# Kernel tuning notes

Measured on AMD Instinct MI355X. Metric: run time of the kernel, lower is better.

## Reference

```python
import jax, jax.numpy as jnp
import numpy as np

N_NODES = 50000
N_EDGES = 640000
IN_DIM = 128
HID = 256
OUT = 256
BN_EPS = 1e-5
L2_EPS = 1e-12


def setup_inputs() -> dict:
    key = jax.random.key(0)
    ks = jax.random.split(key, 12)
    x = jax.random.normal(ks[0], (N_NODES, IN_DIM), dtype=jnp.float32)
    edge_index = jax.random.randint(ks[1], (2, N_EDGES), 0, N_NODES, dtype=jnp.int64)
    s0 = 1.0 / np.sqrt(IN_DIM)
    s1 = 1.0 / np.sqrt(HID)
    return {
        "x": x,
        "edge_index": edge_index,
        # SAGEConv layer 0: lin_l (aggregated neighbors, with bias), lin_r (root, no bias)
        "W_l0": jax.random.uniform(ks[2], (IN_DIM, HID), jnp.float32, -s0, s0),
        "b_l0": jax.random.uniform(ks[3], (HID,), jnp.float32, -s0, s0),
        "W_r0": jax.random.uniform(ks[4], (IN_DIM, HID), jnp.float32, -s0, s0),
        # SAGEConv layer 1
        "W_l1": jax.random.uniform(ks[5], (HID, OUT), jnp.float32, -s1, s1),
        "b_l1": jax.random.uniform(ks[6], (OUT,), jnp.float32, -s1, s1),
        "W_r1": jax.random.uniform(ks[7], (HID, OUT), jnp.float32, -s1, s1),
        # BatchNorm1d (eval mode: running stats)
        "bn_gamma": jax.random.uniform(ks[8], (HID,), jnp.float32, 0.5, 1.5),
        "bn_beta": 0.1 * jax.random.normal(ks[9], (HID,), dtype=jnp.float32),
        "bn_mean": 0.1 * jax.random.normal(ks[10], (HID,), dtype=jnp.float32),
        "bn_var": jax.random.uniform(ks[11], (HID,), jnp.float32, 0.5, 1.5),
    }


def _l2norm(v):
    # F.normalize(v, p=2, dim=1)
    n = jnp.sqrt(jnp.sum(v * v, axis=1, keepdims=True))
    return v / jnp.maximum(n, L2_EPS)


def _sage_mean(x, src, dst, W_l, b_l, W_r, n_nodes):
    # mean-aggregate source features at destination nodes (PyG source_to_target)
    msg = x[src]                                   # [E, d] gather
    agg = jax.ops.segment_sum(msg, dst, num_segments=n_nodes)
    cnt = jax.ops.segment_sum(jnp.ones((src.shape[0], 1), x.dtype), dst, num_segments=n_nodes)
    agg = agg / jnp.maximum(cnt, 1.0)
    out = agg @ W_l + b_l + x @ W_r
    return _l2norm(out)                            # SAGEConv(normalize=True)


def reference(x, edge_index, W_l0, b_l0, W_r0, W_l1, b_l1, W_r1,
              bn_gamma, bn_beta, bn_mean, bn_var):
    src, dst = edge_index[0], edge_index[1]
    n = x.shape[0]
    h = _sage_mean(x, src, dst, W_l0, b_l0, W_r0, n)
    # BatchNorm1d in eval mode (dropout is identity in eval)
    h = (h - bn_mean) * (bn_gamma / jnp.sqrt(bn_var + BN_EPS)) + bn_beta
    h = jax.nn.relu(h)
    h = _sage_mean(h, src, dst, W_l1, b_l1, W_r1, n)
    # final F.normalize(x, p=2, dim=1)
    return _l2norm(h)
```

## Files before the change

### kernel.cpp

```cpp
#include <hip/hip_runtime.h>

#define NN 50000

typedef __bf16 bf16x8 __attribute__((ext_vector_type(8)));
typedef float f32x4 __attribute__((ext_vector_type(4)));
typedef float f32x2 __attribute__((ext_vector_type(2)));

__device__ __forceinline__ unsigned short f2bf(float f) {
    unsigned int u = __builtin_bit_cast(unsigned int, f);
    u += 0x7FFF + ((u >> 16) & 1);
    return (unsigned short)(u >> 16);
}
__device__ __forceinline__ float bf2f(unsigned short h) {
    unsigned int u = ((unsigned int)h) << 16;
    return __builtin_bit_cast(float, u);
}
__device__ __forceinline__ unsigned char f2fp8(float f) {
    return (unsigned char)(__builtin_amdgcn_cvt_pk_fp8_f32(f, f, 0, false) & 0xff);
}
__device__ __forceinline__ void gload16(const void* g, void* l) {
    __builtin_amdgcn_global_load_lds(
        (const __attribute__((address_space(1))) unsigned int*)g,
        (__attribute__((address_space(3))) unsigned int*)l, 16, 0, 0);
}

__global__ void init_kernel(const int* __restrict__ ei32, int* __restrict__ flag,
                            int* __restrict__ cnt, int n) {
    if (blockIdx.x == 0) {
        __shared__ int red[256];
        int tid = threadIdx.x;
        int o = 0;
        for (int i = tid; i < 4096; i += 256) o |= ei32[2 * i + 1];
        red[tid] = o;
        __syncthreads();
        for (int s = 128; s > 0; s >>= 1) {
            if (tid < s) red[tid] |= red[tid + s];
            __syncthreads();
        }
        if (tid == 0) *flag = (red[0] == 0) ? 1 : 0;
    } else {
        int i0 = (blockIdx.x - 1) * 1024 + threadIdx.x * 4;
#pragma unroll
        for (int j = 0; j < 4; ++j) {
            int i = i0 + j;
            if (i < n) cnt[i] = 0;
        }
    }
}

__device__ __forceinline__ int load_edge(const void* ei, int is64, long long idx) {
    return is64 ? (int)((const long long*)ei)[idx] : ((const int*)ei)[idx];
}

__global__ void hist_kernel(const void* __restrict__ ei, const int* __restrict__ flag,
                            int* __restrict__ cnt, int E) {
    int e = blockIdx.x * blockDim.x + threadIdx.x;
    if (e >= E) return;
    int is64 = *flag;
    int dst = load_edge(ei, is64, (long long)E + e);
    atomicAdd(&cnt[dst], 1);
}

__global__ void scan_part(const int* __restrict__ cnt, int* __restrict__ bsum, int n) {
    __shared__ int s[256];
    const int tid = threadIdx.x;
    const int i0 = blockIdx.x * 1024 + tid * 4;
    int sum = 0;
#pragma unroll
    for (int j = 0; j < 4; ++j) {
        int i = i0 + j;
        if (i < n) sum += cnt[i];
    }
    s[tid] = sum;
    __syncthreads();
    for (int o = 128; o > 0; o >>= 1) {
        if (tid < o) s[tid] += s[tid + o];
        __syncthreads();
    }
    if (tid == 0) bsum[blockIdx.x] = s[0];
}

__global__ void scan_fin2(const int* __restrict__ cnt, const int* __restrict__ bsum,
                          int* __restrict__ off, int* __restrict__ pos, int n, int nb) {
    __shared__ int s[256];
    __shared__ int base_sh, total_sh;
    const int tid = threadIdx.x;
    if (tid < 64) {
        int v = (tid < nb) ? bsum[tid] : 0;
        int incl = v;
#pragma unroll
        for (int o = 1; o < 64; o <<= 1) {
            int t = __shfl_up(incl, o, 64);
            if (tid >= o) incl += t;
        }
        if (tid == (int)blockIdx.x) base_sh = incl - v;
        if (tid == 63) total_sh = incl;
    }
    const int i0 = blockIdx.x * 1024 + tid * 4;
    int v[4];
    int sum = 0;
#pragma unroll
    for (int j = 0; j < 4; ++j) {
        int i = i0 + j;
        v[j] = (i < n) ? cnt[i] : 0;
        sum += v[j];
    }
    s[tid] = sum;
    __syncthreads();
    for (int o = 1; o < 256; o <<= 1) {
        int t = 0;
        if (tid >= o) t = s[tid - o];
        __syncthreads();
        s[tid] += t;
        __syncthreads();
    }
    int run = base_sh + s[tid] - sum;
#pragma unroll
    for (int j = 0; j < 4; ++j) {
        int i = i0 + j;
        if (i < n) {
            off[i] = run;
            pos[i] = run;
            run += v[j];
        }
    }
    if (blockIdx.x == 0 && tid == 0) off[n] = total_sh;
}

__global__ void fill_kernel(const void* __restrict__ ei, const int* __restrict__ flag,
                            int* __restrict__ pos, int* __restrict__ adj, int E) {
    int e = blockIdx.x * blockDim.x + threadIdx.x;
    if (e >= E) return;
    int is64 = *flag;
    int src = load_edge(ei, is64, e);
    int dst = load_edge(ei, is64, (long long)E + e);
    int p = atomicAdd(&pos[dst], 1);
    adj[p] = src;
}

__global__ void prep_fused(const float* __restrict__ x, unsigned char* __restrict__ xf8,
                           unsigned short* __restrict__ xbf_t,
                           const float* __restrict__ Wl0, const float* __restrict__ Wr0,
                           unsigned short* __restrict__ Wt0,
                           const float* __restrict__ Wl1, const float* __restrict__ Wr1,
                           unsigned short* __restrict__ Wt1, int n4, int NC) {
    int b = blockIdx.x;
    if (b < NC) {
        int i = b * 256 + threadIdx.x;
        if (i >= n4) return;
        float4 v = ((const float4*)x)[i];
        int p8 = __builtin_amdgcn_cvt_pk_fp8_f32(v.x, v.y, 0, false);
        p8 = __builtin_amdgcn_cvt_pk_fp8_f32(v.z, v.w, p8, true);
        ((unsigned int*)xf8)[i] = (unsigned int)p8;
        uint2 o;
        o.x = (unsigned int)f2bf(v.x) | ((unsigned int)f2bf(v.y) << 16);
        o.y = (unsigned int)f2bf(v.z) | ((unsigned int)f2bf(v.w) << 16);
        int r = i >> 5;
        int kk = (i & 31) * 4;
        int ts = kk >> 5, q = (kk >> 3) & 3, e = kk & 7;
        size_t idx = ((size_t)(r >> 6) * 4 + ts) * 2048 + q * 512 + (r & 63) * 8 + e;
        *(uint2*)(xbf_t + idx) = o;
    } else if (b < NC + 256) {
        int c = b - NC;
        for (int k = threadIdx.x; k < 256; k += blockDim.x) {
            float v = (k < 128) ? Wl0[(size_t)k * 256 + c] : Wr0[(size_t)(k - 128) * 256 + c];
            int ks = k >> 5, q = (k >> 3) & 3, e = k & 7;
            Wt0[(size_t)ks * 8192 + q * 2048 + c * 8 + e] = f2bf(v);
        }
    } else {
        int c = b - NC - 256;
        for (int k = threadIdx.x; k < 512; k += blockDim.x) {
            float v = (k < 256) ? Wl1[(size_t)k * 256 + c] : Wr1[(size_t)(k - 256) * 256 + c];
            int ks = k >> 5, q = (k >> 3) & 3, e = k & 7;
            Wt1[(size_t)ks * 8192 + q * 2048 + c * 8 + e] = f2bf(v);
        }
    }
}

__global__ void agg_l0(const unsigned char* __restrict__ feat8, const int* __restrict__ off,
                       const int* __restrict__ adj, unsigned short* __restrict__ out_t, int n) {
    int node = blockIdx.x * 8 + (threadIdx.x >> 5);
    if (node >= n) return;
    const int lane = threadIdx.x & 31;
    const int s = off[node], e = off[node + 1];

    float a0[4] = {}, a1[4] = {}, a2[4] = {}, a3[4] = {};
    const unsigned char* fbase = feat8 + lane * 4;

    auto addrow = [&](float* acc, int src) {
        unsigned int u = *(const unsigned int*)(fbase + (size_t)src * 128);
        f32x2 lo = __builtin_amdgcn_cvt_pk_f32_fp8(u, false);
        f32x2 hi = __builtin_amdgcn_cvt_pk_f32_fp8(u, true);
        acc[0] += lo[0];
        acc[1] += lo[1];
        acc[2] += hi[0];
        acc[3] += hi[1];
    };

    int j = s;
    for (; j + 4 <= e; j += 4) {
        int i0 = adj[j], i1 = adj[j + 1], i2 = adj[j + 2], i3 = adj[j + 3];
        addrow(a0, i0);
        addrow(a1, i1);
        addrow(a2, i2);
        addrow(a3, i3);
    }
    {
        int rem = e - j;
        if (rem > 0) addrow(a0, adj[j]);
        if (rem > 1) addrow(a1, adj[j + 1]);
        if (rem > 2) addrow(a2, adj[j + 2]);
    }

    int deg = e - s;
    float inv = 1.0f / (float)(deg > 0 ? deg : 1);
#pragma unroll
    for (int k = 0; k < 4; ++k) a0[k] = (a0[k] + a1[k] + a2[k] + a3[k]) * inv;

    const int k0 = lane * 4;
    const int ts = k0 >> 5, q = (k0 >> 3) & 3, e8 = k0 & 7;
    size_t idx = ((size_t)(node >> 6) * 4 + ts) * 2048 + q * 512 + (node & 63) * 8 + e8;
    uint2 o;
    o.x = (unsigned int)f2bf(a0[0]) | ((unsigned int)f2bf(a0[1]) << 16);
    o.y = (unsigned int)f2bf(a0[2]) | ((unsigned int)f2bf(a0[3]) << 16);
    *(uint2*)(out_t + idx) = o;
}

__global__ void agg_l1(const unsigned char* __restrict__ feat8, const int* __restrict__ off,
                       const int* __restrict__ adj, unsigned short* __restrict__ out_t, int n) {
    int node = blockIdx.x * 8 + (threadIdx.x >> 5);
    if (node >= n) return;
    const int lane = threadIdx.x & 31;
    const int s = off[node], e = off[node + 1];

    float a0[8] = {}, a1[8] = {}, a2[8] = {}, a3[8] = {};
    const unsigned char* fbase = feat8 + lane * 8;

    auto addrow = [&](float* acc, int src) {
        uint2 u = *(const uint2*)(fbase + (size_t)src * 256);
        f32x2 p0 = __builtin_amdgcn_cvt_pk_f32_fp8(u.x, false);
        f32x2 p1 = __builtin_amdgcn_cvt_pk_f32_fp8(u.x, true);
        f32x2 p2 = __builtin_amdgcn_cvt_pk_f32_fp8(u.y, false);
        f32x2 p3 = __builtin_amdgcn_cvt_pk_f32_fp8(u.y, true);
        acc[0] += p0[0];
        acc[1] += p0[1];
        acc[2] += p1[0];
        acc[3] += p1[1];
        acc[4] += p2[0];
        acc[5] += p2[1];
        acc[6] += p3[0];
        acc[7] += p3[1];
    };

    int j = s;
    for (; j + 4 <= e; j += 4) {
        int i0 = adj[j], i1 = adj[j + 1], i2 = adj[j + 2], i3 = adj[j + 3];
        addrow(a0, i0);
        addrow(a1, i1);
        addrow(a2, i2);
        addrow(a3, i3);
    }
    {
        int rem = e - j;
        if (rem > 0) addrow(a0, adj[j]);
        if (rem > 1) addrow(a1, adj[j + 1]);
        if (rem > 2) addrow(a2, adj[j + 2]);
    }

    int deg = e - s;
    float inv = 1.0f / (float)(deg > 0 ? deg : 1);
#pragma unroll
    for (int k = 0; k < 8; ++k) a0[k] = (a0[k] + a1[k] + a2[k] + a3[k]) * inv;

    const int k0 = lane * 8;
    const int ts = k0 >> 5, q = (k0 >> 3) & 3;
    size_t idx = ((size_t)(node >> 6) * 8 + ts) * 2048 + q * 512 + (node & 63) * 8;
    uint4 o;
    o.x = (unsigned int)f2bf(a0[0]) | ((unsigned int)f2bf(a0[1]) << 16);
    o.y = (unsigned int)f2bf(a0[2]) | ((unsigned int)f2bf(a0[3]) << 16);
    o.z = (unsigned int)f2bf(a0[4]) | ((unsigned int)f2bf(a0[5]) << 16);
    o.w = (unsigned int)f2bf(a0[6]) | ((unsigned int)f2bf(a0[7]) << 16);
    *(uint4*)(out_t + idx) = o;
}

template <int KH, bool L0>
__device__ __forceinline__ void sage_body(
    unsigned char (*a_sh)[4096], unsigned char (*b_sh)[16384],
    float (*red)[64], float* inv_sh,
    const unsigned short* __restrict__ Aagg_t, const unsigned short* __restrict__ Axin_t,
    const unsigned short* __restrict__ WtT, const float* __restrict__ bl,
    const float* __restrict__ bng, const float* __restrict__ bnb,
    const float* __restrict__ bnm, const float* __restrict__ bnv,
    unsigned char* __restrict__ hout8, unsigned short* __restrict__ hout_t,
    float* __restrict__ fout, int n) {
    constexpr int NSTEP = (2 * KH) / 32;
    constexpr int NAT = KH / 32;

    const int tid = threadIdx.x;
    const int w = tid >> 6;
    const int l = tid & 63;
    const int g = l >> 4;
    const int li = l & 15;
    const int row0 = blockIdx.x * 64;
    const int blk = blockIdx.x;

    f32x4 acc[4][4];
#pragma unroll
    for (int m = 0; m < 4; ++m)
#pragma unroll
        for (int nn = 0; nn < 4; ++nn) acc[m][nn] = (f32x4)(0.0f);

    auto stage = [&](int buf, int t) {
        const unsigned short* at =
            (t < NAT) ? Aagg_t + ((size_t)blk * NAT + t) * 2048
                      : Axin_t + ((size_t)blk * NAT + (t - NAT)) * 2048;
        gload16((const char*)at + w * 1024 + l * 16, &a_sh[buf][w * 1024]);
#pragma unroll
        for (int q = 0; q < 4; ++q)
            gload16((const char*)(WtT + (size_t)t * 8192) + q * 4096 + w * 1024 + l * 16,
                    &b_sh[buf][q * 4096 + w * 1024]);
    };

    auto compute = [&](int buf) {
        bf16x8 bfr[4];
#pragma unroll
        for (int nn = 0; nn < 4; ++nn)
            bfr[nn] = __builtin_bit_cast(
                bf16x8, *(const uint4*)&b_sh[buf][g * 4096 + (w * 64 + nn * 16 + li) * 16]);
        bf16x8 afr[4];
#pragma unroll
        for (int m = 0; m < 4; ++m)
            afr[m] = __builtin_bit_cast(bf16x8, *(const uint4*)&a_sh[buf][g * 1024 + (16 * m + li) * 16]);
#pragma unroll
        for (int nn = 0; nn < 4; ++nn)
#pragma unroll
            for (int m = 0; m < 4; ++m)
                acc[m][nn] = __builtin_amdgcn_mfma_f32_16x16x32_bf16(afr[m], bfr[nn], acc[m][nn], 0, 0, 0);
    };

    stage(0, 0);
    __syncthreads();

    int cur = 0;
    for (int ks = 0; ks < NSTEP - 1; ++ks) {
        stage(cur ^ 1, ks + 1);
        asm volatile("s_waitcnt vmcnt(5)" ::: "memory");
        __builtin_amdgcn_sched_barrier(0);
        __builtin_amdgcn_s_barrier();
        __builtin_amdgcn_sched_barrier(0);
        compute(cur);
        __builtin_amdgcn_s_barrier();
        __builtin_amdgcn_sched_barrier(0);
        cur ^= 1;
    }
    asm volatile("s_waitcnt vmcnt(0)" ::: "memory");
    __builtin_amdgcn_sched_barrier(0);
    __builtin_amdgcn_s_barrier();
    __builtin_amdgcn_sched_barrier(0);
    compute(cur);

    float bv[4];
#pragma unroll
    for (int nn = 0; nn < 4; ++nn) bv[nn] = bl[w * 64 + nn * 16 + li];
#pragma unroll
    for (int m = 0; m < 4; ++m)
#pragma unroll
        for (int nn = 0; nn < 4; ++nn)
#pragma unroll
            for (int r = 0; r < 4; ++r) acc[m][nn][r] += bv[nn];

    float ssp[4][4];
#pragma unroll
    for (int m = 0; m < 4; ++m)
#pragma unroll
        for (int r = 0; r < 4; ++r) {
            float s = 0.f;
#pragma unroll
            for (int nn = 0; nn < 4; ++nn) s += acc[m][nn][r] * acc[m][nn][r];
#pragma unroll
            for (int mk = 1; mk < 16; mk <<= 1) s += __shfl_xor(s, mk, 64);
            ssp[m][r] = s;
        }
    __syncthreads();
    if (li == 0) {
#pragma unroll
        for (int m = 0; m < 4; ++m)
#pragma unroll
            for (int r = 0; r < 4; ++r) red[w][16 * m + 4 * g + r] = ssp[m][r];
    }
    __syncthreads();
    if (tid < 64) {
        float tot = red[0][tid] + red[1][tid] + red[2][tid] + red[3][tid];
        inv_sh[tid] = 1.0f / fmaxf(sqrtf(tot), 1e-12f);
    }
    __syncthreads();

    float sc[4], sh[4];
    if (L0) {
#pragma unroll
        for (int nn = 0; nn < 4; ++nn) {
            int c = w * 64 + nn * 16 + li;
            float s = bng[c] * rsqrtf(bnv[c] + 1e-5f);
            sc[nn] = s;
            sh[nn] = bnb[c] - bnm[c] * s;
        }
    }
#pragma unroll
    for (int m = 0; m < 4; ++m) {
#pragma unroll
        for (int r = 0; r < 4; ++r) {
            int rl = 16 * m + 4 * g + r;
            int row = row0 + rl;
            if (row < n) {
                float inv = inv_sh[rl];
#pragma unroll
                for (int nn = 0; nn < 4; ++nn) {
                    int c = w * 64 + nn * 16 + li;
                    float v = acc[m][nn][r] * inv;
                    if (L0) {
                        v = fmaxf(v * sc[nn] + sh[nn], 0.f);
                        hout8[(size_t)row * 256 + c] = f2fp8(v);
                        int ts = c >> 5, q = (c >> 3) & 3, e8 = c & 7;
                        hout_t[((size_t)(row >> 6) * 8 + ts) * 2048 + q * 512 + (row & 63) * 8 + e8] =
                            f2bf(v);
                    } else {
                        fout[(size_t)row * 256 + c] = v;
                    }
                }
            }
        }
    }
}

__global__ void gemm_l0(const unsigned short* __restrict__ Aagg_t,
                        const unsigned short* __restrict__ Axin_t,
                        const unsigned short* __restrict__ WtT, const float* __restrict__ bl,
                        const float* __restrict__ bng, const float* __restrict__ bnb,
                        const float* __restrict__ bnm, const float* __restrict__ bnv,
                        unsigned char* __restrict__ hout8, unsigned short* __restrict__ hout_t,
                        int n) {
    __shared__ __align__(16) unsigned char a_sh[2][4096];
    __shared__ __align__(16) unsigned char b_sh[2][16384];
    __shared__ float red[4][64];
    __shared__ float inv_sh[64];
    sage_body<128, true>(a_sh, b_sh, red, inv_sh, Aagg_t, Axin_t, WtT, bl, bng, bnb, bnm, bnv,
                         hout8, hout_t, nullptr, n);
}

__global__ void gemm_l1(const unsigned short* __restrict__ Aagg_t,
                        const unsigned short* __restrict__ Axin_t,
                        const unsigned short* __restrict__ WtT, const float* __restrict__ bl,
                        float* __restrict__ fout, int n) {
    __shared__ __align__(16) unsigned char a_sh[2][4096];
    __shared__ __align__(16) unsigned char b_sh[2][16384];
    __shared__ float red[4][64];
    __shared__ float inv_sh[64];
    sage_body<256, false>(a_sh, b_sh, red, inv_sh, Aagg_t, Axin_t, WtT, bl, nullptr, nullptr,
                          nullptr, nullptr, nullptr, nullptr, fout, n);
}

extern "C" void kernel_launch(void* const* d_in, const int* in_sizes, int n_in,
                              void* d_out, int out_size, void* d_ws, size_t ws_size,
                              hipStream_t stream) {
    const float* x   = (const float*)d_in[0];
    const void*  ei  = d_in[1];
    const float* Wl0 = (const float*)d_in[2];
    const float* bl0 = (const float*)d_in[3];
    const float* Wr0 = (const float*)d_in[4];
    const float* Wl1 = (const float*)d_in[5];
    const float* bl1 = (const float*)d_in[6];
    const float* Wr1 = (const float*)d_in[7];
    const float* bng = (const float*)d_in[8];
    const float* bnb = (const float*)d_in[9];
    const float* bnm = (const float*)d_in[10];
    const float* bnv = (const float*)d_in[11];
    float* out = (float*)d_out;

    const int N = NN;
    const int E = in_sizes[1] / 2;
    const int NB = (N + 1023) / 1024;
    const int NBK = (N + 63) / 64;

    char* wsp = (char*)d_ws;
    size_t o = 0;
    auto carve = [&](size_t bytes) {
        void* p = wsp + o;
        o = (o + bytes + 255) & ~(size_t)255;
        return p;
    };
    int* flag = (int*)carve(4);
    int* cnt  = (int*)carve((size_t)N * 4);
    int* off  = (int*)carve((size_t)(N + 1) * 4);
    int* pos  = (int*)carve((size_t)N * 4);
    int* bsum = (int*)carve((size_t)NB * 4);
    int* adj  = (int*)carve((size_t)E * 4);
    unsigned char*  xf8  = (unsigned char*)carve((size_t)N * 128);
    unsigned char*  hf8  = (unsigned char*)carve((size_t)N * 256);
    unsigned short* big  = (unsigned short*)carve((size_t)NBK * 8 * 2048 * 2);
    unsigned short* xbf_t  = big;
    unsigned short* agg0_t = big + (size_t)NBK * 4 * 2048;
    unsigned short* agg1_t = big;
    unsigned short* hbf_t  = (unsigned short*)carve((size_t)NBK * 8 * 2048 * 2);
    unsigned short* Wt0  = (unsigned short*)carve((size_t)8 * 8192 * 2);
    unsigned short* Wt1  = (unsigned short*)carve((size_t)16 * 8192 * 2);

    init_kernel<<<1 + NB, 256, 0, stream>>>((const int*)ei, flag, cnt, N);
    hist_kernel<<<(E + 255) / 256, 256, 0, stream>>>(ei, flag, cnt, E);
    scan_part<<<NB, 256, 0, stream>>>(cnt, bsum, N);
    scan_fin2<<<NB, 256, 0, stream>>>(cnt, bsum, off, pos, N, NB);
    fill_kernel<<<(E + 255) / 256, 256, 0, stream>>>(ei, flag, pos, adj, E);

    const int n4 = N * 128 / 4;
    const int NC = (n4 + 255) / 256;
    prep_fused<<<NC + 512, 256, 0, stream>>>(x, xf8, xbf_t, Wl0, Wr0, Wt0, Wl1, Wr1, Wt1,
                                             n4, NC);

    agg_l0<<<(N + 7) / 8, 256, 0, stream>>>(xf8, off, adj, agg0_t, N);
    gemm_l0<<<NBK, 256, 0, stream>>>(agg0_t, xbf_t, Wt0, bl0, bng, bnb, bnm, bnv,
                                     hf8, hbf_t, N);

    agg_l1<<<(N + 7) / 8, 256, 0, stream>>>(hf8, off, adj, agg1_t, N);
    gemm_l1<<<NBK, 256, 0, stream>>>(agg1_t, hbf_t, Wt1, bl1, out, N);
}
```

Before: 200.9 us.

## Fuse neighbor aggregation into SAGE GEMM kernels via shared-memory A tile

The mean aggregation is moved into the GEMM kernels. Each 64-row block gathers neighbor fp8 features, averages them, and writes the bf16 aggregate straight into LDS, so the aggregated matrix never makes a round trip through global memory. The GEMM pipeline is split into an agg phase, which reads A from LDS, and a root phase, which streams A from global. Separately, the CSR fill and the prep kernel are merged into one launch to cut launch count. The cost is more LDS per block (up to 32KB extra for layer 1), which lowers occupancy. Aggregation parallelism also drops to one block per 64 nodes, with the gather latency serialized before the MFMA work.

```diff
diff --git a/kernel.cpp b/kernel.cpp
--- a/kernel.cpp
+++ b/kernel.cpp
@@ -10,10 +10,6 @@
     unsigned int u = __builtin_bit_cast(unsigned int, f);
     u += 0x7FFF + ((u >> 16) & 1);
     return (unsigned short)(u >> 16);
-}
-__device__ __forceinline__ float bf2f(unsigned short h) {
-    unsigned int u = ((unsigned int)h) << 16;
-    return __builtin_bit_cast(float, u);
 }
 __device__ __forceinline__ unsigned char f2fp8(float f) {
     return (unsigned char)(__builtin_amdgcn_cvt_pk_fp8_f32(f, f, 0, false) & 0xff);
@@ -127,26 +123,25 @@
     if (blockIdx.x == 0 && tid == 0) off[n] = total_sh;
 }
 
-__global__ void fill_kernel(const void* __restrict__ ei, const int* __restrict__ flag,
-                            int* __restrict__ pos, int* __restrict__ adj, int E) {
-    int e = blockIdx.x * blockDim.x + threadIdx.x;
-    if (e >= E) return;
-    int is64 = *flag;
-    int src = load_edge(ei, is64, e);
-    int dst = load_edge(ei, is64, (long long)E + e);
-    int p = atomicAdd(&pos[dst], 1);
-    adj[p] = src;
-}
-
-__global__ void prep_fused(const float* __restrict__ x, unsigned char* __restrict__ xf8,
-                           unsigned short* __restrict__ xbf_t,
-                           const float* __restrict__ Wl0, const float* __restrict__ Wr0,
-                           unsigned short* __restrict__ Wt0,
-                           const float* __restrict__ Wl1, const float* __restrict__ Wr1,
-                           unsigned short* __restrict__ Wt1, int n4, int NC) {
+__global__ void fill_prep(const void* __restrict__ ei, const int* __restrict__ flag,
+                          int* __restrict__ pos, int* __restrict__ adj, int E, int EB,
+                          const float* __restrict__ x, unsigned char* __restrict__ xf8,
+                          unsigned short* __restrict__ xbf_t,
+                          const float* __restrict__ Wl0, const float* __restrict__ Wr0,
+                          unsigned short* __restrict__ Wt0,
+                          const float* __restrict__ Wl1, const float* __restrict__ Wr1,
+                          unsigned short* __restrict__ Wt1, int n4, int NC) {
     int b = blockIdx.x;
-    if (b < NC) {
-        int i = b * 256 + threadIdx.x;
+    if (b < EB) {
+        int e = b * 256 + threadIdx.x;
+        if (e >= E) return;
+        int is64 = *flag;
+        int src = load_edge(ei, is64, e);
+        int dst = load_edge(ei, is64, (long long)E + e);
+        int p = atomicAdd(&pos[dst], 1);
+        adj[p] = src;
+    } else if (b < EB + NC) {
+        int i = (b - EB) * 256 + threadIdx.x;
         if (i >= n4) return;
         float4 v = ((const float4*)x)[i];
         int p8 = __builtin_amdgcn_cvt_pk_fp8_f32(v.x, v.y, 0, false);
@@ -160,15 +155,15 @@
         int ts = kk >> 5, q = (kk >> 3) & 3, e = kk & 7;
         size_t idx = ((size_t)(r >> 6) * 4 + ts) * 2048 + q * 512 + (r & 63) * 8 + e;
         *(uint2*)(xbf_t + idx) = o;
-    } else if (b < NC + 256) {
-        int c = b - NC;
+    } else if (b < EB + NC + 256) {
+        int c = b - EB - NC;
         for (int k = threadIdx.x; k < 256; k += blockDim.x) {
             float v = (k < 128) ? Wl0[(size_t)k * 256 + c] : Wr0[(size_t)(k - 128) * 256 + c];
             int ks = k >> 5, q = (k >> 3) & 3, e = k & 7;
             Wt0[(size_t)ks * 8192 + q * 2048 + c * 8 + e] = f2bf(v);
         }
     } else {
-        int c = b - NC - 256;
+        int c = b - EB - NC - 256;
         for (int k = threadIdx.x; k < 512; k += blockDim.x) {
             float v = (k < 256) ? Wl1[(size_t)k * 256 + c] : Wr1[(size_t)(k - 256) * 256 + c];
             int ks = k >> 5, q = (k >> 3) & 3, e = k & 7;
@@ -177,117 +172,12 @@
     }
 }
 
-__global__ void agg_l0(const unsigned char* __restrict__ feat8, const int* __restrict__ off,
-                       const int* __restrict__ adj, unsigned short* __restrict__ out_t, int n) {
-    int node = blockIdx.x * 8 + (threadIdx.x >> 5);
-    if (node >= n) return;
-    const int lane = threadIdx.x & 31;
-    const int s = off[node], e = off[node + 1];
-
-    float a0[4] = {}, a1[4] = {}, a2[4] = {}, a3[4] = {};
-    const unsigned char* fbase = feat8 + lane * 4;
-
-    auto addrow = [&](float* acc, int src) {
-        unsigned int u = *(const unsigned int*)(fbase + (size_t)src * 128);
-        f32x2 lo = __builtin_amdgcn_cvt_pk_f32_fp8(u, false);
-        f32x2 hi = __builtin_amdgcn_cvt_pk_f32_fp8(u, true);
-        acc[0] += lo[0];
-        acc[1] += lo[1];
-        acc[2] += hi[0];
-        acc[3] += hi[1];
-    };
-
-    int j = s;
-    for (; j + 4 <= e; j += 4) {
-        int i0 = adj[j], i1 = adj[j + 1], i2 = adj[j + 2], i3 = adj[j + 3];
-        addrow(a0, i0);
-        addrow(a1, i1);
-        addrow(a2, i2);
-        addrow(a3, i3);
-    }
-    {
-        int rem = e - j;
-        if (rem > 0) addrow(a0, adj[j]);
-        if (rem > 1) addrow(a1, adj[j + 1]);
-        if (rem > 2) addrow(a2, adj[j + 2]);
-    }
-
-    int deg = e - s;
-    float inv = 1.0f / (float)(deg > 0 ? deg : 1);
-#pragma unroll
-    for (int k = 0; k < 4; ++k) a0[k] = (a0[k] + a1[k] + a2[k] + a3[k]) * inv;
-
-    const int k0 = lane * 4;
-    const int ts = k0 >> 5, q = (k0 >> 3) & 3, e8 = k0 & 7;
-    size_t idx = ((size_t)(node >> 6) * 4 + ts) * 2048 + q * 512 + (node & 63) * 8 + e8;
-    uint2 o;
-    o.x = (unsigned int)f2bf(a0[0]) | ((unsigned int)f2bf(a0[1]) << 16);
-    o.y = (unsigned int)f2bf(a0[2]) | ((unsigned int)f2bf(a0[3]) << 16);
-    *(uint2*)(out_t + idx) = o;
-}
-
-__global__ void agg_l1(const unsigned char* __restrict__ feat8, const int* __restrict__ off,
-                       const int* __restrict__ adj, unsigned short* __restrict__ out_t, int n) {
-    int node = blockIdx.x * 8 + (threadIdx.x >> 5);
-    if (node >= n) return;
-    const int lane = threadIdx.x & 31;
-    const int s = off[node], e = off[node + 1];
-
-    float a0[8] = {}, a1[8] = {}, a2[8] = {}, a3[8] = {};
-    const unsigned char* fbase = feat8 + lane * 8;
-
-    auto addrow = [&](float* acc, int src) {
-        uint2 u = *(const uint2*)(fbase + (size_t)src * 256);
-        f32x2 p0 = __builtin_amdgcn_cvt_pk_f32_fp8(u.x, false);
-        f32x2 p1 = __builtin_amdgcn_cvt_pk_f32_fp8(u.x, true);
-        f32x2 p2 = __builtin_amdgcn_cvt_pk_f32_fp8(u.y, false);
-        f32x2 p3 = __builtin_amdgcn_cvt_pk_f32_fp8(u.y, true);
-        acc[0] += p0[0];
-        acc[1] += p0[1];
-        acc[2] += p1[0];
-        acc[3] += p1[1];
-        acc[4] += p2[0];
-        acc[5] += p2[1];
-        acc[6] += p3[0];
-        acc[7] += p3[1];
-    };
-
-    int j = s;
-    for (; j + 4 <= e; j += 4) {
-        int i0 = adj[j], i1 = adj[j + 1], i2 = adj[j + 2], i3 = adj[j + 3];
-        addrow(a0, i0);
-        addrow(a1, i1);
-        addrow(a2, i2);
-        addrow(a3, i3);
-    }
-    {
-        int rem = e - j;
-        if (rem > 0) addrow(a0, adj[j]);
-        if (rem > 1) addrow(a1, adj[j + 1]);
-        if (rem > 2) addrow(a2, adj[j + 2]);
-    }
-
-    int deg = e - s;
-    float inv = 1.0f / (float)(deg > 0 ? deg : 1);
-#pragma unroll
-    for (int k = 0; k < 8; ++k) a0[k] = (a0[k] + a1[k] + a2[k] + a3[k]) * inv;
-
-    const int k0 = lane * 8;
-    const int ts = k0 >> 5, q = (k0 >> 3) & 3;
-    size_t idx = ((size_t)(node >> 6) * 8 + ts) * 2048 + q * 512 + (node & 63) * 8;
-    uint4 o;
-    o.x = (unsigned int)f2bf(a0[0]) | ((unsigned int)f2bf(a0[1]) << 16);
-    o.y = (unsigned int)f2bf(a0[2]) | ((unsigned int)f2bf(a0[3]) << 16);
-    o.z = (unsigned int)f2bf(a0[4]) | ((unsigned int)f2bf(a0[5]) << 16);
-    o.w = (unsigned int)f2bf(a0[6]) | ((unsigned int)f2bf(a0[7]) << 16);
-    *(uint4*)(out_t + idx) = o;
-}
-
 template <int KH, bool L0>
-__device__ __forceinline__ void sage_body(
-    unsigned char (*a_sh)[4096], unsigned char (*b_sh)[16384],
+__device__ __forceinline__ void sage_fused_body(
+    unsigned short* A_agg, unsigned char (*a_sh)[4096], unsigned char (*b_sh)[16384],
     float (*red)[64], float* inv_sh,
-    const unsigned short* __restrict__ Aagg_t, const unsigned short* __restrict__ Axin_t,
+    const unsigned char* __restrict__ feat8, const int* __restrict__ off,
+    const int* __restrict__ adj, const unsigned short* __restrict__ Axin_t,
     const unsigned short* __restrict__ WtT, const float* __restrict__ bl,
     const float* __restrict__ bng, const float* __restrict__ bnb,
     const float* __restrict__ bnm, const float* __restrict__ bnv,
@@ -304,51 +194,181 @@
     const int row0 = blockIdx.x * 64;
     const int blk = blockIdx.x;
 
-    f32x4 acc[4][4];
-#pragma unroll
-    for (int m = 0; m < 4; ++m)
-#pragma unroll
-        for (int nn = 0; nn < 4; ++nn) acc[m][nn] = (f32x4)(0.0f);
-
-    auto stage = [&](int buf, int t) {
-        const unsigned short* at =
-            (t < NAT) ? Aagg_t + ((size_t)blk * NAT + t) * 2048
-                      : Axin_t + ((size_t)blk * NAT + (t - NAT)) * 2048;
-        gload16((const char*)at + w * 1024 + l * 16, &a_sh[buf][w * 1024]);
+    auto stageB = [&](int buf, int t) {
 #pragma unroll
         for (int q = 0; q < 4; ++q)
             gload16((const char*)(WtT + (size_t)t * 8192) + q * 4096 + w * 1024 + l * 16,
                     &b_sh[buf][q * 4096 + w * 1024]);
     };
-
-    auto compute = [&](int buf) {
-        bf16x8 bfr[4];
+    auto stageA = [&](int buf, int t) {
+        const unsigned short* at = Axin_t + ((size_t)blk * NAT + (t - NAT)) * 2048;
+        gload16((const char*)at + w * 1024 + l * 16, &a_sh[buf][w * 1024]);
+    };
+
+    stageB(0, 0);
+
+    {
+        const int hw = tid >> 5;
+        const int lane = tid & 31;
+        for (int r8 = 0; r8 < 8; ++r8) {
+            int node = row0 + r8 * 8 + hw;
+            if (node >= n) continue;
+            const int s = off[node], e = off[node + 1];
+            const int row = node & 63;
+            if constexpr (L0) {
+                float a0[4] = {}, a1[4] = {}, a2[4] = {}, a3[4] = {};
+                const unsigned char* fb = feat8 + lane * 4;
+                auto addrow = [&](float* acc, int src) {
+                    unsigned int u = *(const unsigned int*)(fb + (size_t)src * 128);
+                    f32x2 lo = __builtin_amdgcn_cvt_pk_f32_fp8(u, false);
+                    f32x2 hi = __builtin_amdgcn_cvt_pk_f32_fp8(u, true);
+                    acc[0] += lo[0];
+                    acc[1] += lo[1];
+                    acc[2] += hi[0];
+                    acc[3] += hi[1];
+                };
+                int j = s;
+                for (; j + 4 <= e; j += 4) {
+                    int i0 = adj[j], i1 = adj[j + 1], i2 = adj[j + 2], i3 = adj[j + 3];
+                    addrow(a0, i0);
+                    addrow(a1, i1);
+                    addrow(a2, i2);
+                    addrow(a3, i3);
+                }
+                int rem = e - j;
+                if (rem > 0) addrow(a0, adj[j]);
+                if (rem > 1) addrow(a1, adj[j + 1]);
+                if (rem > 2) addrow(a2, adj[j + 2]);
+                int deg = e - s;
+                float inv = 1.0f / (float)(deg > 0 ? deg : 1);
+#pragma unroll
+                for (int k2 = 0; k2 < 4; ++k2) a0[k2] = (a0[k2] + a1[k2] + a2[k2] + a3[k2]) * inv;
+                const int k0 = lane * 4;
+                const int ts = k0 >> 5, q = (k0 >> 3) & 3, e8 = k0 & 7;
+                uint2 o;
+                o.x = (unsigned int)f2bf(a0[0]) | ((unsigned int)f2bf(a0[1]) << 16);
+                o.y = (unsigned int)f2bf(a0[2]) | ((unsigned int)f2bf(a0[3]) << 16);
+                *(uint2*)&A_agg[ts * 2048 + q * 512 + row * 8 + e8] = o;
+            } else {
+                float a0[8] = {}, a1[8] = {}, a2[8] = {}, a3[8] = {};
+                const unsigned char* fb = feat8 + lane * 8;
+                auto addrow = [&](float* acc, int src) {
+                    uint2 u = *(const uint2*)(fb + (size_t)src * 256);
+                    f32x2 p0 = __builtin_amdgcn_cvt_pk_f32_fp8(u.x, false);
+                    f32x2 p1 = __builtin_amdgcn_cvt_pk_f32_fp8(u.x, true);
+                    f32x2 p2 = __builtin_amdgcn_cvt_pk_f32_fp8(u.y, false);
+                    f32x2 p3 = __builtin_amdgcn_cvt_pk_f32_fp8(u.y, true);
+                    acc[0] += p0[0];
+                    acc[1] += p0[1];
+                    acc[2] += p1[0];
+                    acc[3] += p1[1];
+                    acc[4] += p2[0];
+                    acc[5] += p2[1];
+                    acc[6] += p3[0];
+                    acc[7] += p3[1];
+                };
+                int j = s;
+                for (; j + 4 <= e; j += 4) {
+                    int i0 = adj[j], i1 = adj[j + 1], i2 = adj[j + 2], i3 = adj[j + 3];
+                    addrow(a0, i0);
+                    addrow(a1, i1);
+                    addrow(a2, i2);
+                    addrow(a3, i3);
+                }
+                int rem = e - j;
+                if (rem > 0) addrow(a0, adj[j]);
+                if (rem > 1) addrow(a1, adj[j + 1]);
+                if (rem > 2) addrow(a2, adj[j + 2]);
+                int deg = e - s;
+                float inv = 1.0f / (float)(deg > 0 ? deg : 1);
+#pragma unroll
+                for (int k2 = 0; k2 < 8; ++k2) a0[k2] = (a0[k2] + a1[k2] + a2[k2] + a3[k2]) * inv;
+                const int k0 = lane * 8;
+                const int ts = k0 >> 5, q = (k0 >> 3) & 3;
+                uint4 o;
+                o.x = (unsigned int)f2bf(a0[0]) | ((unsigned int)f2bf(a0[1]) << 16);
+                o.y = (unsigned int)f2bf(a0[2]) | ((unsigned int)f2bf(a0[3]) << 16);
+                o.z = (unsigned int)f2bf(a0[4]) | ((unsigned int)f2bf(a0[5]) << 16);
+                o.w = (unsigned int)f2bf(a0[6]) | ((unsigned int)f2bf(a0[7]) << 16);
+                *(uint4*)&A_agg[ts * 2048 + q * 512 + row * 8] = o;
+            }
+        }
+    }
+    __syncthreads();
+
+    f32x4 acc[4][4];
+#pragma unroll
+    for (int m = 0; m < 4; ++m)
+#pragma unroll
+        for (int nn = 0; nn < 4; ++nn) acc[m][nn] = (f32x4)(0.0f);
+
+    auto mfma16 = [&](const bf16x8* afr, const bf16x8* bfr) {
+#pragma unroll
+        for (int nn = 0; nn < 4; ++nn)
+#pragma unroll
+            for (int m = 0; m < 4; ++m)
+                acc[m][nn] = __builtin_amdgcn_mfma_f32_16x16x32_bf16(afr[m], bfr[nn], acc[m][nn], 0, 0, 0);
+    };
+    auto loadB = [&](int buf, bf16x8* bfr) {
 #pragma unroll
         for (int nn = 0; nn < 4; ++nn)
             bfr[nn] = __builtin_bit_cast(
                 bf16x8, *(const uint4*)&b_sh[buf][g * 4096 + (w * 64 + nn * 16 + li) * 16]);
+    };
+    auto computeAgg = [&](int buf, int step) {
+        bf16x8 bfr[4];
+        loadB(buf, bfr);
+        bf16x8 afr[4];
+#pragma unroll
+        for (int m = 0; m < 4; ++m)
+            afr[m] = __builtin_bit_cast(
+                bf16x8,
+                *(const uint4*)((const unsigned char*)A_agg + (size_t)step * 4096 + g * 1024 +
+                                (16 * m + li) * 16));
+        mfma16(afr, bfr);
+    };
+    auto computeXin = [&](int buf) {
+        bf16x8 bfr[4];
+        loadB(buf, bfr);
         bf16x8 afr[4];
 #pragma unroll
         for (int m = 0; m < 4; ++m)
             afr[m] = __builtin_bit_cast(bf16x8, *(const uint4*)&a_sh[buf][g * 1024 + (16 * m + li) * 16]);
-#pragma unroll
-        for (int nn = 0; nn < 4; ++nn)
-#pragma unroll
-            for (int m = 0; m < 4; ++m)
-                acc[m][nn] = __builtin_amdgcn_mfma_f32_16x16x32_bf16(afr[m], bfr[nn], acc[m][nn], 0, 0, 0);
-    };
-
-    stage(0, 0);
-    __syncthreads();
+        mfma16(afr, bfr);
+    };
 
     int cur = 0;
-    for (int ks = 0; ks < NSTEP - 1; ++ks) {
-        stage(cur ^ 1, ks + 1);
+    for (int ks = 0; ks < NAT - 1; ++ks) {
+        stageB(cur ^ 1, ks + 1);
+        asm volatile("s_waitcnt vmcnt(4)" ::: "memory");
+        __builtin_amdgcn_sched_barrier(0);
+        __builtin_amdgcn_s_barrier();
+        __builtin_amdgcn_sched_barrier(0);
+        computeAgg(cur, ks);
+        __builtin_amdgcn_s_barrier();
+        __builtin_amdgcn_sched_barrier(0);
+        cur ^= 1;
+    }
+    {
+        stageB(cur ^ 1, NAT);
+        stageA(cur ^ 1, NAT);
         asm volatile("s_waitcnt vmcnt(5)" ::: "memory");
         __builtin_amdgcn_sched_barrier(0);
         __builtin_amdgcn_s_barrier();
         __builtin_amdgcn_sched_barrier(0);
-        compute(cur);
+        computeAgg(cur, NAT - 1);
+        __builtin_amdgcn_s_barrier();
+        __builtin_amdgcn_sched_barrier(0);
+        cur ^= 1;
+    }
+    for (int ks = NAT; ks < NSTEP - 1; ++ks) {
+        stageB(cur ^ 1, ks + 1);
+        stageA(cur ^ 1, ks + 1);
+        asm volatile("s_waitcnt vmcnt(5)" ::: "memory");
+        __builtin_amdgcn_sched_barrier(0);
+        __builtin_amdgcn_s_barrier();
+        __builtin_amdgcn_sched_barrier(0);
+        computeXin(cur);
         __builtin_amdgcn_s_barrier();
         __builtin_amdgcn_sched_barrier(0);
         cur ^= 1;
@@ -357,7 +377,7 @@
     __builtin_amdgcn_sched_barrier(0);
     __builtin_amdgcn_s_barrier();
     __builtin_amdgcn_sched_barrier(0);
-    compute(cur);
+    computeXin(cur);
 
     float bv[4];
 #pragma unroll
@@ -432,31 +452,33 @@
     }
 }
 
-__global__ void gemm_l0(const unsigned short* __restrict__ Aagg_t,
-                        const unsigned short* __restrict__ Axin_t,
-                        const unsigned short* __restrict__ WtT, const float* __restrict__ bl,
-                        const float* __restrict__ bng, const float* __restrict__ bnb,
-                        const float* __restrict__ bnm, const float* __restrict__ bnv,
-                        unsigned char* __restrict__ hout8, unsigned short* __restrict__ hout_t,
-                        int n) {
+__global__ void gemm_l0f(const unsigned char* __restrict__ xf8, const int* __restrict__ off,
+                         const int* __restrict__ adj, const unsigned short* __restrict__ xbf_t,
+                         const unsigned short* __restrict__ Wt0, const float* __restrict__ bl,
+                         const float* __restrict__ bng, const float* __restrict__ bnb,
+                         const float* __restrict__ bnm, const float* __restrict__ bnv,
+                         unsigned char* __restrict__ hf8, unsigned short* __restrict__ hbf_t,
+                         int n) {
+    __shared__ __align__(16) unsigned short A_agg[4 * 2048];
     __shared__ __align__(16) unsigned char a_sh[2][4096];
     __shared__ __align__(16) unsigned char b_sh[2][16384];
     __shared__ float red[4][64];
     __shared__ float inv_sh[64];
-    sage_body<128, true>(a_sh, b_sh, red, inv_sh, Aagg_t, Axin_t, WtT, bl, bng, bnb, bnm, bnv,
-                         hout8, hout_t, nullptr, n);
-}
-
-__global__ void gemm_l1(const unsigned short* __restrict__ Aagg_t,
-                        const unsigned short* __restrict__ Axin_t,
-                        const unsigned short* __restrict__ WtT, const float* __restrict__ bl,
-                        float* __restrict__ fout, int n) {
+    sage_fused_body<128, true>(A_agg, a_sh, b_sh, red, inv_sh, xf8, off, adj, xbf_t, Wt0, bl,
+                               bng, bnb, bnm, bnv, hf8, hbf_t, nullptr, n);
+}
+
+__global__ void gemm_l1f(const unsigned char* __restrict__ hf8, const int* __restrict__ off,
+                         const int* __restrict__ adj, const unsigned short* __restrict__ hbf_t,
+                         const unsigned short* __restrict__ Wt1, const float* __restrict__ bl,
+                         float* __restrict__ fout, int n) {
+    __shared__ __align__(16) unsigned short A_agg[8 * 2048];
     __shared__ __align__(16) unsigned char a_sh[2][4096];
     __shared__ __align__(16) unsigned char b_sh[2][16384];
     __shared__ float red[4][64];
     __shared__ float inv_sh[64];
-    sage_body<256, false>(a_sh, b_sh, red, inv_sh, Aagg_t, Axin_t, WtT, bl, nullptr, nullptr,
-                          nullptr, nullptr, nullptr, nullptr, fout, n);
+    sage_fused_body<256, false>(A_agg, a_sh, b_sh, red, inv_sh, hf8, off, adj, hbf_t, Wt1, bl,
+                                nullptr, nullptr, nullptr, nullptr, nullptr, nullptr, fout, n);
 }
 
 extern "C" void kernel_launch(void* const* d_in, const int* in_sizes, int n_in,
@@ -480,6 +502,7 @@
     const int E = in_sizes[1] / 2;
     const int NB = (N + 1023) / 1024;
     const int NBK = (N + 63) / 64;
+    const int EB = (E + 255) / 256;
 
     char* wsp = (char*)d_ws;
     size_t o = 0;
@@ -496,29 +519,22 @@
     int* adj  = (int*)carve((size_t)E * 4);
     unsigned char*  xf8  = (unsigned char*)carve((size_t)N * 128);
     unsigned char*  hf8  = (unsigned char*)carve((size_t)N * 256);
-    unsigned short* big  = (unsigned short*)carve((size_t)NBK * 8 * 2048 * 2);
-    unsigned short* xbf_t  = big;
-    unsigned short* agg0_t = big + (size_t)NBK * 4 * 2048;
-    unsigned short* agg1_t = big;
-    unsigned short* hbf_t  = (unsigned short*)carve((size_t)NBK * 8 * 2048 * 2);
+    unsigned short* xbf_t = (unsigned short*)carve((size_t)NBK * 4 * 2048 * 2);
+    unsigned short* hbf_t = (unsigned short*)carve((size_t)NBK * 8 * 2048 * 2);
     unsigned short* Wt0  = (unsigned short*)carve((size_t)8 * 8192 * 2);
     unsigned short* Wt1  = (unsigned short*)carve((size_t)16 * 8192 * 2);
 
     init_kernel<<<1 + NB, 256, 0, stream>>>((const int*)ei, flag, cnt, N);
-    hist_kernel<<<(E + 255) / 256, 256, 0, stream>>>(ei, flag, cnt, E);
+    hist_kernel<<<EB, 256, 0, stream>>>(ei, flag, cnt, E);
     scan_part<<<NB, 256, 0, stream>>>(cnt, bsum, N);
     scan_fin2<<<NB, 256, 0, stream>>>(cnt, bsum, off, pos, N, NB);
-    fill_kernel<<<(E + 255) / 256, 256, 0, stream>>>(ei, flag, pos, adj, E);
 
     const int n4 = N * 128 / 4;
     const int NC = (n4 + 255) / 256;
-    prep_fused<<<NC + 512, 256, 0, stream>>>(x, xf8, xbf_t, Wl0, Wr0, Wt0, Wl1, Wr1, Wt1,
-                                             n4, NC);
-
-    agg_l0<<<(N + 7) / 8, 256, 0, stream>>>(xf8, off, adj, agg0_t, N);
-    gemm_l0<<<NBK, 256, 0, stream>>>(agg0_t, xbf_t, Wt0, bl0, bng, bnb, bnm, bnv,
-                                     hf8, hbf_t, N);
-
-    agg_l1<<<(N + 7) / 8, 256, 0, stream>>>(hf8, off, adj, agg1_t, N);
-    gemm_l1<<<NBK, 256, 0, stream>>>(agg1_t, hbf_t, Wt1, bl1, out, N);
-}
+    fill_prep<<<EB + NC + 512, 256, 0, stream>>>(ei, flag, pos, adj, E, EB, x, xf8, xbf_t,
+                                                 Wl0, Wr0, Wt0, Wl1, Wr1, Wt1, n4, NC);
+
+    gemm_l0f<<<NBK, 256, 0, stream>>>(xf8, off, adj, xbf_t, Wt0, bl0, bng, bnb, bnm, bnv,
+                                      hf8, hbf_t, N);
+    gemm_l1f<<<NBK, 256, 0, stream>>>(hf8, off, adj, hbf_t, Wt1, bl1, out, N);
+}
```

After: 261.5 us. +30.2%, slower.
